# Kernel tuning notes

Hardware: AMD Instinct MI355X
Metric: run time of the kernel (lower is better)

## Reference

```python
import jax, jax.numpy as jnp
import numpy as np
from jax import lax
from jax.scipy.special import gammaln

B, T_FEATS, T_TEXT = 16, 2000, 400
ADIM, ODIM = 256, 512
BIG_NEG = -1e30
BLANK_LOGP = -1.0  # log(blank_prob) with blank_prob = e**-1


def _conv1d(x, w, b, pad):
    # x: (B, C_in, L), w: (C_out, C_in, K)
    y = lax.conv_general_dilated(x, w, (1,), [(pad, pad)],
                                 dimension_numbers=('NCH', 'OIH', 'NCH'))
    return y + b[None, :, None]


def _betabinom_prior(T, N):
    # ESPnet AlignmentModule beta-binomial attention prior (w=1):
    # alpha_t = t (1..T), beta_t = T - t + 1, k = 1..N, n = N
    t = jnp.arange(1, T + 1, dtype=jnp.float32)
    a = t[:, None]                                   # (T,1)
    bb = (T - t + 1.0)[:, None]                      # (T,1)
    k = jnp.arange(1, N + 1, dtype=jnp.float32)[None, :]  # (1,N)
    n = float(N)
    betaln = lambda x, y: gammaln(x) + gammaln(y) - gammaln(x + y)
    logC = gammaln(n + 1.0) - gammaln(k + 1.0) - gammaln(n - k + 1.0)
    return logC + betaln(k + a, n - k + bb) - betaln(a, bb)  # (T,N)


def _alignment_encoder(txt, speech, tw1, tb1, tw2, tb2, fw1, fb1, fw2, fb2, fw3, fb3):
    t = txt.transpose(0, 2, 1)                       # (B, adim, T_text)
    t = jax.nn.relu(_conv1d(t, tw1, tb1, 1))
    t = _conv1d(t, tw2, tb2, 0)
    t = t.transpose(0, 2, 1)                         # (B, T_text, adim)

    f = speech.transpose(0, 2, 1)                    # (B, odim, T_feats)
    f = jax.nn.relu(_conv1d(f, fw1, fb1, 1))
    f = jax.nn.relu(_conv1d(f, fw2, fb2, 1))
    f = _conv1d(f, fw3, fb3, 0)
    f = f.transpose(0, 2, 1)                         # (B, T_feats, adim)

    # score = -||f_t - t_s||_2 via expansion (avoids (B,T,S,D) intermediate)
    d2 = (jnp.sum(f * f, -1)[:, :, None] + jnp.sum(t * t, -1)[:, None, :]
          - 2.0 * jnp.einsum('btd,bsd->bts', f, t))
    score = -jnp.sqrt(jnp.maximum(d2, 1e-12))        # (B, T_feats, T_text)
    logp = jax.nn.log_softmax(score, axis=-1)
    return logp + _betabinom_prior(T_FEATS, T_TEXT)[None]


def _forwardsum_loss(log_p_attn):
    # CTC forward algorithm; targets are 1..N (all distinct) + interleaved blanks
    Bv, T, N = log_p_attn.shape
    lp = jnp.concatenate(
        [jnp.full((Bv, T, 1), BLANK_LOGP, log_p_attn.dtype), log_p_attn], axis=-1)
    lp = jax.nn.log_softmax(lp, axis=-1)             # (B, T, N+1)
    S = 2 * N + 1
    ext = np.zeros(S, np.int32); ext[1::2] = np.arange(1, N + 1)
    skip_ok = np.zeros(S, bool); skip_ok[3::2] = True  # non-blank, distinct labels
    ext = jnp.asarray(ext); skip_ok = jnp.asarray(skip_ok)

    emit = lp[:, :, ext]                             # (B, T, S)
    alpha = jnp.full((Bv, S), BIG_NEG)
    alpha = alpha.at[:, 0].set(emit[:, 0, 0]).at[:, 1].set(emit[:, 0, 1])

    def step(alpha, e):
        a1 = jnp.concatenate([jnp.full((Bv, 1), BIG_NEG), alpha[:, :-1]], axis=1)
        a2 = jnp.concatenate([jnp.full((Bv, 2), BIG_NEG), alpha[:, :-2]], axis=1)
        a2 = jnp.where(skip_ok[None, :], a2, BIG_NEG)
        alpha = jnp.logaddexp(jnp.logaddexp(alpha, a1), a2) + e
        return alpha, None

    alpha, _ = lax.scan(step, alpha, jnp.moveaxis(emit[:, 1:], 1, 0))
    nll = -jnp.logaddexp(alpha[:, -1], alpha[:, -2])  # (B,)
    # F.ctc_loss reduction='mean' divides each sample's nll by target length
    return jnp.mean(nll / N)


def _mas_single(lp):
    # lp: (T_feats, T_text) -> monotonic alignment (T_feats,) int32
    log_prob = lp.T                                  # (N, T)
    N, T = T_TEXT, T_FEATS
    q0 = jnp.where(jnp.arange(N) == 0, log_prob[0, 0], BIG_NEG)

    def fwd(q, col):
        q = jnp.maximum(q, jnp.concatenate([jnp.full((1,), BIG_NEG), q[:-1]])) + col
        return q, q

    _, qs = lax.scan(fwd, q0, log_prob[:, 1:].T)     # (T-1, N)
    Q = lax.stop_gradient(jnp.concatenate([q0[None], qs], axis=0))  # (T, N)

    def bwd(a_next, q_col):
        i_a = jnp.maximum(a_next - 1, 0)
        a = jnp.where(a_next == 0, 0,
                      jnp.where(q_col[i_a] >= q_col[a_next], i_a, a_next))
        a = a.astype(jnp.int32)
        return a, a

    _, A_rev = lax.scan(bwd, jnp.array(N - 1, jnp.int32), Q[:-1], reverse=True)
    return jnp.concatenate([A_rev, jnp.array([N - 1], jnp.int32)])  # (T,)


def _viterbi_decode(log_p_attn):
    A = jax.vmap(_mas_single)(log_p_attn)            # (B, T_feats) int32
    ds = jax.vmap(lambda a: jnp.bincount(a, length=T_TEXT))(A)
    ds = ds.astype(log_p_attn.dtype)                 # (B, T_text) durations
    gathered = jnp.take_along_axis(log_p_attn, A[:, :, None], axis=2)[..., 0]
    bin_loss = -jnp.mean(jnp.mean(gathered, axis=1))
    return ds, bin_loss


def setup_inputs() -> dict:
    key = jax.random.key(0)
    ks = jax.random.split(key, 12)
    s = 0.05
    inp = {
        'speech': jax.random.normal(ks[0], (B, T_FEATS, ODIM), jnp.float32),
        'txt': jax.random.normal(ks[1], (B, T_TEXT, ADIM), jnp.float32),
        'speech_len': jnp.full((B,), T_FEATS, jnp.int32),
        'txt_len': jnp.full((B,), T_TEXT, jnp.int32),
        'tw1': jax.random.normal(ks[2], (ADIM, ADIM, 3)) * s,
        'tb1': jnp.zeros((ADIM,)),
        'tw2': jax.random.normal(ks[3], (ADIM, ADIM, 1)) * s,
        'tb2': jnp.zeros((ADIM,)),
        'fw1': jax.random.normal(ks[4], (ADIM, ODIM, 3)) * s,
        'fb1': jnp.zeros((ADIM,)),
        'fw2': jax.random.normal(ks[5], (ADIM, ADIM, 3)) * s,
        'fb2': jnp.zeros((ADIM,)),
        'fw3': jax.random.normal(ks[6], (ADIM, ADIM, 1)) * s,
        'fb3': jnp.zeros((ADIM,)),
    }
    return inp


def reference(speech, txt, speech_len, txt_len,
              tw1, tb1, tw2, tb2, fw1, fb1, fw2, fb2, fw3, fb3):
    # lengths are full (no padding), so masks are no-ops
    log_p_attn = _alignment_encoder(txt, speech, tw1, tb1, tw2, tb2,
                                    fw1, fb1, fw2, fb2, fw3, fb3)
    forwardsum_loss = _forwardsum_loss(log_p_attn)
    ds, bin_loss = _viterbi_decode(log_p_attn)
    return ds, bin_loss, forwardsum_loss, log_p_attn
```

## Files before the change

### kernel.cpp

```cpp
#include <hip/hip_runtime.h>
#include <math.h>

typedef unsigned int u32;
typedef unsigned long long u64;
typedef unsigned short u16;
typedef __attribute__((ext_vector_type(8))) _Float16 f16x8;
typedef __attribute__((ext_vector_type(4))) float f32x4;

#define BIGN (-1e30f)

static constexpr int NB = 16;
static constexpr int TF = 2000;
static constexpr int TT = 400;

__device__ __forceinline__ float wsum(float v){
#pragma unroll
  for(int o=32;o;o>>=1) v += __shfl_xor(v,o,64);
  return v;
}
__device__ __forceinline__ float EXP2(float x){ return __builtin_amdgcn_exp2f(x); }
__device__ __forceinline__ float LOG2(float x){ return __builtin_amdgcn_logf(x); }
__device__ __forceinline__ float lse2b(float x, float y){
  float m = fmaxf(x,y);
  return m + LOG2(1.0f + EXP2(-fabsf(x-y)));
}
__device__ __forceinline__ float lse3b(float x, float y, float z){
  float mx = fmaxf(fmaxf(x,y),z);
  float md = __builtin_amdgcn_fmed3f(x,y,z);
  float mn = fminf(fminf(x,y),z);
  return mx + LOG2(1.0f + EXP2(md-mx) + EXP2(mn-mx));
}
__device__ __forceinline__ u16 f2h(float v){
  _Float16 h = (_Float16)v;
  return *(u16*)&h;
}
__device__ __forceinline__ float shup1(float v){
  int r = __builtin_amdgcn_update_dpp(__float_as_int(BIGN), __float_as_int(v),
                                      0x138, 0xf, 0xf, false);
  return __int_as_float(r);
}

__global__ void k_lgt(double* lgt){
  int m = blockIdx.x*blockDim.x + threadIdx.x;
  if(m < 2432) lgt[m] = (m>=1)? lgamma((double)m) : 0.0;
}
__global__ void k_terms(const double* __restrict__ lgt, double* rowA, double* colA, double* sA){
  int i = blockIdx.x*blockDim.x + threadIdx.x;
  if(i < TF)   rowA[i] = -lgt[2401] - lgt[i+1] - lgt[2000-i] + lgt[2001];
  if(i < TT)   colA[i] =  lgt[401]  - lgt[i+2] - lgt[400-i];
  if(i < 2399) sA[i]   =  lgt[i+2]  + lgt[2399-i];
}

__device__ __forceinline__ void packf(const float* __restrict__ w, u16* __restrict__ dst,
    int CIN, int KW, int i){
  int k = i % KW;
  int c = (i / KW) % CIN;
  int o = i / (KW*CIN);
  dst[((size_t)k*256 + o)*CIN + c] = f2h(w[i]);
}
__device__ __forceinline__ void cvtp(const float* __restrict__ src, u16* __restrict__ dst,
    int P, int C, int i){
  int c = i % C;
  int p = (i / C) % (P+2);
  int b = i / (C*(P+2));
  float v = 0.f;
  if(p>=1 && p<=P) v = src[((size_t)b*P + (p-1))*C + c];
  dst[i] = f2h(v);
}
__device__ __forceinline__ void zpr(u16* __restrict__ buf, int P, int j){
  int c = j % 256;
  int s = (j / 256) & 1;
  int b = j / 512;
  buf[((size_t)b*(P+2) + (s? P+1 : 0))*256 + c] = 0;
}
__global__ __launch_bounds__(256) void prep1_k(
    const float* __restrict__ fw1, const float* __restrict__ fw2, const float* __restrict__ fw3,
    const float* __restrict__ tw1, const float* __restrict__ tw2, const float* __restrict__ txt,
    u16* fw1p, u16* fw2p, u16* fw3p, u16* tw1p, u16* tw2p,
    u16* inbfT, u16* tout1, u16* out1){
  constexpr int N = 393216+196608+65536+196608+65536+1646592+8192+8192;
  for(int i = blockIdx.x*256 + threadIdx.x; i < N; i += gridDim.x*256){
    int j = i;
    if(j < 393216){ packf(fw1, fw1p, 512, 3, j); continue; } j -= 393216;
    if(j < 196608){ packf(fw2, fw2p, 256, 3, j); continue; } j -= 196608;
    if(j < 65536) { packf(fw3, fw3p, 256, 1, j); continue; } j -= 65536;
    if(j < 196608){ packf(tw1, tw1p, 256, 3, j); continue; } j -= 196608;
    if(j < 65536) { packf(tw2, tw2p, 256, 1, j); continue; } j -= 65536;
    if(j < 1646592){ cvtp(txt, inbfT, TT, 256, j); continue; } j -= 1646592;
    if(j < 8192) { zpr(tout1, TT, j); continue; } j -= 8192;
    zpr(out1, TF, j);
  }
}

__global__ __launch_bounds__(256) void cvt_pad_k(const float* __restrict__ src, u16* __restrict__ dst,
    int P, int C){
  int n = NB*(P+2)*C;
  for(int i = blockIdx.x*256 + threadIdx.x; i < n; i += gridDim.x*256) cvtp(src, dst, P, C, i);
}
__global__ __launch_bounds__(256) void zpad_k(u16* __restrict__ buf, int P){
  int n = NB*2*256;
  for(int i = blockIdx.x*256 + threadIdx.x; i < n; i += gridDim.x*256) zpr(buf, P, i);
}

template<int CIN, int KW, bool RELU, bool OBF>
__global__ __launch_bounds__(256) void mfconv_k(const u16* __restrict__ inb,
    const u16* __restrict__ wp, const float* __restrict__ bias, void* __restrict__ outp, int P){
  __shared__ __align__(16) u16 Al[4*66*8];
  __shared__ __align__(16) u16 Bl[KW*4*256*8];
  const int b = blockIdx.y;
  const int m0 = blockIdx.x * 64;
  const int tid = threadIdx.x;
  const int lane = tid & 63, wv = tid >> 6;
  const int lo16 = lane & 15, hi = lane >> 4;
  constexpr int K1 = (KW==1)? 1 : 0;
  const u16* inB = inb + (size_t)b*(P+2)*CIN;
  f32x4 acc[4][4];
#pragma unroll
  for(int i=0;i<4;i++)
#pragma unroll
    for(int j=0;j<4;j++) acc[i][j] = (f32x4){0.f,0.f,0.f,0.f};

  for(int c0=0; c0<CIN; c0+=32){
    __syncthreads();
    for(int idx = tid; idx < 264; idx += 256){
      int r = idx >> 2, q = idx & 3;
      int rowp = m0 + r;
      f16x8 v = (f16x8){0,0,0,0,0,0,0,0};
      if(rowp <= P+1) v = *(const f16x8*)&inB[(size_t)rowp*CIN + c0 + q*8];
      *(f16x8*)&Al[(q*66 + r)*8] = v;
    }
#pragma unroll
    for(int k=0;k<KW;k++){
      const u16* wr = &wp[((size_t)(k*256) + tid)*CIN + c0];
      f16x8 w0 = *(const f16x8*)&wr[0];
      f16x8 w1 = *(const f16x8*)&wr[8];
      f16x8 w2 = *(const f16x8*)&wr[16];
      f16x8 w3 = *(const f16x8*)&wr[24];
      *(f16x8*)&Bl[((k*4+0)*256 + tid)*8] = w0;
      *(f16x8*)&Bl[((k*4+1)*256 + tid)*8] = w1;
      *(f16x8*)&Bl[((k*4+2)*256 + tid)*8] = w2;
      *(f16x8*)&Bl[((k*4+3)*256 + tid)*8] = w3;
    }
    __syncthreads();
#pragma unroll
    for(int k=0;k<KW;k++){
      f16x8 af[4];
#pragma unroll
      for(int rf=0;rf<4;rf++)
        af[rf] = *(const f16x8*)&Al[(hi*66 + rf*16 + lo16 + k + K1)*8];
#pragma unroll
      for(int cf=0;cf<4;cf++){
        int o = wv*64 + cf*16 + lo16;
        f16x8 bf = *(const f16x8*)&Bl[((k*4+hi)*256 + o)*8];
#pragma unroll
        for(int rf=0;rf<4;rf++)
          acc[rf][cf] = __builtin_amdgcn_mfma_f32_16x16x32_f16(af[rf], bf, acc[rf][cf], 0, 0, 0);
      }
    }
  }
#pragma unroll
  for(int cf=0;cf<4;cf++){
    int o = wv*64 + cf*16 + lo16;
    float bs = bias[o];
#pragma unroll
    for(int rf=0;rf<4;rf++){
#pragma unroll
      for(int j=0;j<4;j++){
        int p = m0 + rf*16 + hi*4 + j;
        if(p < P){
          float v = acc[rf][cf][j] + bs;
          if(RELU) v = fmaxf(v, 0.f);
          if(OBF) ((u16*)outp)[((size_t)b*(P+2) + p + 1)*256 + o] = f2h(v);
          else    ((float*)outp)[((size_t)b*P + p)*256 + o] = v;
        }
      }
    }
  }
}

__global__ __launch_bounds__(256) void norm2b_k(const float* __restrict__ x1, const float* __restrict__ x2,
    float* __restrict__ o1, float* __restrict__ o2){
  int r = blockIdx.x*4 + (threadIdx.x>>6);
  int lane = threadIdx.x & 63;
  const float* src; float* dst; int rr;
  if(r < NB*TF){ src = x1; dst = o1; rr = r; }
  else { rr = r - NB*TF; if(rr >= NB*TT) return; src = x2; dst = o2; }
  float4 v = ((const float4*)(src + (size_t)rr*256))[lane];
  float s = v.x*v.x + v.y*v.y + v.z*v.z + v.w*v.w;
  s = wsum(s);
  if(lane==0) dst[rr] = s;
}

__global__ __launch_bounds__(256) void score_gemm(const float* __restrict__ F, const float* __restrict__ Tn,
    const float* __restrict__ fn2, const float* __restrict__ tn2, float* __restrict__ outp){
  constexpr int KC = 32;
  __shared__ __align__(16) float As[KC][68];
  __shared__ __align__(16) float Bs[KC][68];
  const int b = blockIdx.z;
  const int t0 = blockIdx.y*64, s0 = blockIdx.x*64;
  const int tid = threadIdx.x, tx = tid&15, ty = tid>>4;
  const float* Fb = F  + (size_t)b*TF*256;
  const float* Tb = Tn + (size_t)b*TT*256;
  float acc[4][4] = {};
  const int lk = tid & 31, lt0 = (tid>>5)*8;
  for(int k0=0;k0<256;k0+=KC){
    __syncthreads();
#pragma unroll
    for(int i=0;i<8;i++){
      int t = t0 + lt0 + i;
      As[lk][lt0+i] = (t<TF)? Fb[(size_t)t*256 + k0 + lk] : 0.f;
      int s = s0 + lt0 + i;
      Bs[lk][lt0+i] = (s<TT)? Tb[(size_t)s*256 + k0 + lk] : 0.f;
    }
    __syncthreads();
#pragma unroll
    for(int k=0;k<KC;k++){
      float a0[4], b0[4];
      *(float4*)a0 = *(const float4*)&As[k][ty*4];
      *(float4*)b0 = *(const float4*)&Bs[k][tx*4];
#pragma unroll
      for(int i=0;i<4;i++)
#pragma unroll
        for(int j=0;j<4;j++) acc[i][j] = fmaf(a0[i], b0[j], acc[i][j]);
    }
  }
#pragma unroll
  for(int i=0;i<4;i++){
    int t = t0 + ty*4 + i;
    if(t<TF){
      float fn = fn2[b*TF + t];
#pragma unroll
      for(int j=0;j<4;j++){
        int s = s0 + tx*4 + j;
        if(s<TT){
          float d2 = fn + tn2[b*TT + s] - 2.f*acc[i][j];
          outp[((size_t)b*TF + t)*TT + s] = -sqrtf(fmaxf(d2, 1e-12f));
        }
      }
    }
  }
}

__global__ __launch_bounds__(128) void softmax_prior_k(float* __restrict__ logp,
    const double* __restrict__ rowA, const double* __restrict__ colA, const double* __restrict__ sA,
    float* __restrict__ Z2){
  const int row = blockIdx.x;
  const int t0 = row % TF;
  float* rp = logp + (size_t)row*TT;
  const int tid = threadIdx.x;
  __shared__ float sh2[2];
  float v[4]; int ix[4];
#pragma unroll
  for(int i=0;i<4;i++){ ix[i] = tid + i*128; v[i] = (ix[i]<TT)? rp[ix[i]] : BIGN; }
  float m = fmaxf(fmaxf(v[0],v[1]),fmaxf(v[2],v[3]));
#pragma unroll
  for(int o=32;o;o>>=1) m = fmaxf(m, __shfl_xor(m,o,64));
  if((tid&63)==0) sh2[tid>>6] = m;
  __syncthreads();
  m = fmaxf(sh2[0], sh2[1]);
  float s = 0.f;
#pragma unroll
  for(int i=0;i<4;i++) if(ix[i]<TT) s += __expf(v[i]-m);
  s = wsum(s);
  __syncthreads();
  if((tid&63)==0) sh2[tid>>6] = s;
  __syncthreads();
  s = sh2[0] + sh2[1];
  const float lse = m + __logf(s);
  const double rA = rowA[t0];
  float f[4]; float m2 = BIGN;
#pragma unroll
  for(int i=0;i<4;i++){
    if(ix[i]<TT){
      float pr = (float)(colA[ix[i]] + sA[t0+ix[i]] + rA);
      f[i] = (v[i]-lse) + pr;
      rp[ix[i]] = f[i];
      m2 = fmaxf(m2, f[i]);
    } else f[i] = BIGN;
  }
#pragma unroll
  for(int o=32;o;o>>=1) m2 = fmaxf(m2, __shfl_xor(m2,o,64));
  __syncthreads();
  if((tid&63)==0) sh2[tid>>6] = m2;
  __syncthreads();
  m2 = fmaxf(fmaxf(sh2[0],sh2[1]), -1.0f);
  float s2 = (tid==0)? __expf(-1.0f - m2) : 0.f;
#pragma unroll
  for(int i=0;i<4;i++) if(ix[i]<TT) s2 += __expf(f[i]-m2);
  s2 = wsum(s2);
  __syncthreads();
  if((tid&63)==0) sh2[tid>>6] = s2;
  __syncthreads();
  if(tid==0) Z2[row] = m2 + __logf(sh2[0]+sh2[1]);
}

#define LCTC8(E) { \
  float n1 = shup1(a[7]); \
  float w0 = lse2b(a[0], n1); \
  float w1 = lse2b(a[2], a[1]); \
  float w2 = lse2b(a[4], a[3]); \
  float w3 = lse2b(a[6], a[5]); \
  a[7] = lse2b(a[7], w3) + (E)[3]; \
  a[5] = lse2b(a[5], w2) + (E)[2]; \
  a[3] = lse2b(a[3], w1) + (E)[1]; \
  a[1] = lse2b(a[1], w0) + (E)[0]; \
  a[6] = w3 + EBL; a[4] = w2 + EBL; a[2] = w1 + EBL; a[0] = w0 + EBL; }

#define CPREF4(E, K) { int kk=(K); if(kk>999) kk=999; int row = dir? (TF-1-kk) : kk; \
  const float* rpp = lp + (size_t)row*TT; \
  (E)[0]=rpp[jc[0]]*IL2; (E)[1]=rpp[jc[1]]*IL2; (E)[2]=rpp[jc[2]]*IL2; (E)[3]=rpp[jc[3]]*IL2; }

#define MAS_STEP(E, TIDX) { \
  float n1 = shup1(q[6]); \
  u32 byte = 0; \
  if(lane>0 && n1 >= q[0]) byte |= 1u; \
  if(q[0] >= q[1]) byte |= 2u; \
  if(q[1] >= q[2]) byte |= 4u; \
  if(q[2] >= q[3]) byte |= 8u; \
  if(q[3] >= q[4]) byte |= 16u; \
  if(q[4] >= q[5]) byte |= 32u; \
  if(q[5] >= q[6]) byte |= 64u; \
  cb[(size_t)((TIDX)-1)*64 + lane] = (unsigned char)byte; \
  q[6] = fmaxf(q[6], q[5]) + (E)[6]; \
  q[5] = fmaxf(q[5], q[4]) + (E)[5]; \
  q[4] = fmaxf(q[4], q[3]) + (E)[4]; \
  q[3] = fmaxf(q[3], q[2]) + (E)[3]; \
  q[2] = fmaxf(q[2], q[1]) + (E)[2]; \
  q[1] = fmaxf(q[1], q[0]) + (E)[1]; \
  q[0] = fmaxf(q[0], n1) + (E)[0]; }

#define MPREF(E, ROW) { int rr=(ROW); rr = (rr>TF-1)? (TF-1) : rr; const float* rpp = lp + (size_t)rr*TT; \
  (E)[0]=rpp[jc[0]]; (E)[1]=rpp[jc[1]]; (E)[2]=rpp[jc[2]]; (E)[3]=rpp[jc[3]]; \
  (E)[4]=rpp[jc[4]]; (E)[5]=rpp[jc[5]]; (E)[6]=rpp[jc[6]]; }

__global__ __launch_bounds__(256) __attribute__((amdgpu_waves_per_eu(1,1)))
void scan_k(const float* __restrict__ logp,
    const float* __restrict__ Z2, unsigned char* __restrict__ cmpb, float* __restrict__ nll){
  const int lane = threadIdx.x & 63;
  const int wave = threadIdx.x >> 6;
  constexpr float IL2 = 1.4426950408889634f;
  constexpr float L2  = 0.6931471805599453f;
  if(blockIdx.x < NB){
    const int b = blockIdx.x;
    const float* lp = logp + (size_t)b*TF*TT;
    __shared__ float af[801], ag[801];
    __shared__ float sb[2][2][16];
    const int dir  = wave >> 1;
    const int half = wave & 1;
    const int sbase = half ? 408 : 0;
    double zs = 0.0;
    if(wave==0){
      for(int t=lane; t<TF; t+=64) zs += (double)Z2[b*TF + t];
#pragma unroll
      for(int o=32;o;o>>=1) zs += __shfl_xor(zs, o, 64);
    }
    int jc[4];
#pragma unroll
    for(int i=0;i<4;i++){
      int j = sbase/2 + 4*lane + i;
      if(dir) j = TT-1-j;
      jc[i] = (j < 0)? 0 : ((j > TT-1)? TT-1 : j);
    }
    float a[8];
#pragma unroll
    for(int i=0;i<8;i++) a[i] = BIGN;
    if(half==0 && lane==0){
      a[0] = -1.0f*IL2;
      a[1] = (dir? lp[(size_t)(TF-1)*TT + (TT-1)] : lp[0]) * IL2;
    }
    const float EBL = -1.0f*IL2;
    if(half==0 && (lane==51 || lane==52)){
#pragma unroll
      for(int i=0;i<8;i++) sb[dir][0][(lane-51)*8+i] = a[i];
    }
    float e0[4],e1[4],e2[4],e3[4],e4[4],e5[4],e6[4],e7[4];
    CPREF4(e0,1); CPREF4(e1,2); CPREF4(e2,3); CPREF4(e3,4);
    CPREF4(e4,5); CPREF4(e5,6); CPREF4(e6,7); CPREF4(e7,8);
    __syncthreads();
    int k = 1, kb = 0;
    for(; k + 8 <= 1000; k += 8, kb++){
      if(half && lane < 2){
#pragma unroll
        for(int i=0;i<8;i++) a[i] = sb[dir][kb&1][lane*8+i];
      }
      LCTC8(e0); CPREF4(e0, k+8);
      LCTC8(e1); CPREF4(e1, k+9);
      LCTC8(e2); CPREF4(e2, k+10);
      LCTC8(e3); CPREF4(e3, k+11);
      LCTC8(e4); CPREF4(e4, k+12);
      LCTC8(e5); CPREF4(e5, k+13);
      LCTC8(e6); CPREF4(e6, k+14);
      LCTC8(e7); CPREF4(e7, k+15);
      if(half==0 && (lane==51 || lane==52)){
#pragma unroll
        for(int i=0;i<8;i++) sb[dir][(kb+1)&1][(lane-51)*8+i] = a[i];
      }
      __syncthreads();
    }
    if(half && lane < 2){
#pragma unroll
      for(int i=0;i<8;i++) a[i] = sb[dir][kb&1][lane*8+i];
    }
    for(; k<=999; k++){
      float P[4];
      CPREF4(P, k);
      LCTC8(P);
    }
    float* dst = dir? ag : af;
#pragma unroll
    for(int i=0;i<8;i++){
      int s = sbase + 8*lane + i;
      if(half){ if(s>=424 && s<=800) dst[s] = a[i]; }
      else    { if(s<=423) dst[s] = a[i]; }
    }
    __syncthreads();
    if(wave==0){
      float acc = BIGN;
      for(int s = lane; s <= 800; s += 64){
        float x0 = af[s];
        float x1 = (s>=1)? af[s-1] : BIGN;
        float x2 = ((s&1) && s>=3)? af[s-2] : BIGN;
        float A1 = lse3b(x0,x1,x2);
        acc = lse2b(acc, A1 + ag[800-s]);
      }
#pragma unroll
      for(int o=32;o;o>>=1) acc = lse2b(acc, __shfl_xor(acc,o,64));
      if(lane==0) nll[b] = -((acc*L2) - (float)zs);
    }
  } else {
    if(wave) return;
    const int b = blockIdx.x - NB;
    const float* lp = logp + (size_t)b*TF*TT;
    unsigned char* cb = cmpb + (size_t)b*TF*64;
    int jc[7];
#pragma unroll
    for(int i=0;i<7;i++){ int j = 7*lane + i; jc[i] = (j < TT)? j : (TT-1); }
    float q[7];
#pragma unroll
    for(int i=0;i<7;i++) q[i] = BIGN;
    if(lane==0) q[0] = lp[0];
    float e0[7],e1[7],e2[7],e3[7];
    MPREF(e0,1); MPREF(e1,2); MPREF(e2,3); MPREF(e3,4);
    int t0 = 1;
    for(; t0 + 4 <= TF; t0 += 4){
      MAS_STEP(e0, t0);   MPREF(e0, t0+4);
      MAS_STEP(e1, t0+1); MPREF(e1, t0+5);
      MAS_STEP(e2, t0+2); MPREF(e2, t0+6);
      MAS_STEP(e3, t0+3); MPREF(e3, t0+7);
    }
    for(; t0<TF; t0++){
      float P[7];
      MPREF(P, t0);
      MAS_STEP(P, t0);
    }
    {
      float n1 = shup1(q[6]);
      u32 byte = 0;
      if(lane>0 && n1 >= q[0]) byte |= 1u;
      if(q[0] >= q[1]) byte |= 2u;
      if(q[1] >= q[2]) byte |= 4u;
      if(q[2] >= q[3]) byte |= 8u;
      if(q[3] >= q[4]) byte |= 16u;
      if(q[4] >= q[5]) byte |= 32u;
      if(q[5] >= q[6]) byte |= 64u;
      cb[(size_t)(TF-1)*64 + lane] = (unsigned char)byte;
    }
  }
}

__global__ __launch_bounds__(256) void masback_k(const unsigned char* __restrict__ cmpb,
    const float* __restrict__ logp, float* __restrict__ ds, float* __restrict__ gsum){
  const int b = blockIdx.x;
  const unsigned char* cb = cmpb + (size_t)b*TF*64;
  __shared__ unsigned char bits[500*64];
  __shared__ short Ash[TF];
  __shared__ int cnt[TT];
  __shared__ float ps[4];
  int a = TT-1;
  for(int ch=3; ch>=0; ch--){
    const int tlo = ch*500;
    __syncthreads();
    for(int i=threadIdx.x;i<8000;i+=256) ((u32*)bits)[i] = ((const u32*)(cb + (size_t)tlo*64))[i];
    __syncthreads();
    if(threadIdx.x==0){
      int thi = tlo + 499;
      if(ch==3){ Ash[TF-1] = (short)(TT-1); thi = TF-2; }
      for(int t=thi;t>=tlo;t--){
        if(a > 0){
          unsigned char w = bits[(t-tlo)*64 + a/7];
          a -= (int)((w >> (a%7)) & 1u);
        }
        Ash[t] = (short)a;
      }
    }
  }
  __syncthreads();
  for(int i=threadIdx.x;i<TT;i+=256) cnt[i]=0;
  __syncthreads();
  float part = 0.f;
  const float* lp = logp + (size_t)b*TF*TT;
  for(int t=threadIdx.x;t<TF;t+=256){
    int at = Ash[t];
    atomicAdd(&cnt[at], 1);
    part += lp[(size_t)t*TT + at];
  }
  __syncthreads();
  for(int i=threadIdx.x;i<TT;i+=256) ds[(size_t)b*TT + i] = (float)cnt[i];
  part = wsum(part);
  if((threadIdx.x&63)==0) ps[threadIdx.x>>6] = part;
  __syncthreads();
  if(threadIdx.x==0) gsum[b] = ps[0]+ps[1]+ps[2]+ps[3];
}

__global__ void final_k(const float* __restrict__ nll, const float* __restrict__ gsum, float* __restrict__ out){
  if(threadIdx.x==0 && blockIdx.x==0){
    float fs=0.f, bs=0.f;
    for(int b=0;b<NB;b++){ fs += nll[b] / (float)TT; bs += gsum[b] / (float)TF; }
    out[6400] = -(bs / (float)NB);
    out[6401] = fs / (float)NB;
  }
}

extern "C" void kernel_launch(void* const* d_in, const int* in_sizes, int n_in,
                              void* d_out, int out_size, void* d_ws, size_t ws_size,
                              hipStream_t stream){
  const float* speech = (const float*)d_in[0];
  const float* txt    = (const float*)d_in[1];
  const float* tw1 = (const float*)d_in[4];
  const float* tb1 = (const float*)d_in[5];
  const float* tw2 = (const float*)d_in[6];
  const float* tb2 = (const float*)d_in[7];
  const float* fw1 = (const float*)d_in[8];
  const float* fb1 = (const float*)d_in[9];
  const float* fw2 = (const float*)d_in[10];
  const float* fb2 = (const float*)d_in[11];
  const float* fw3 = (const float*)d_in[12];
  const float* fb3 = (const float*)d_in[13];
  float* out  = (float*)d_out;
  float* ds   = out;
  float* logp = out + 6402;
  char* ws = (char*)d_ws;
  double* lgt  = (double*)(ws + 0);
  double* rowA = (double*)(ws + 20480);
  double* colA = (double*)(ws + 36864);
  double* sA   = (double*)(ws + 40960);
  float*  nll  = (float*)(ws + 61440);
  float*  gsum = (float*)(ws + 61696);
  float*  Z2   = (float*)(ws + 65536);
  float*  fn2  = (float*)(ws + 196608);
  float*  tn2  = (float*)(ws + 327680);
  unsigned char* cmpb = (unsigned char*)(ws + 360448);
  float*  tenc = (float*)(ws + 2408448);
  float*  f1   = (float*)(ws + 8962048);
  if(ws_size < 41730048) return;

  char* lr = (char*)(((uintptr_t)logp + 255) & ~(uintptr_t)255);
  u16* inbfT = (u16*)lr;
  u16* tout1 = (u16*)(lr + 4000000);
  u16* inbfA = (u16*)lr;
  u16* out2  = (u16*)lr;
  u16* wbase = (u16*)(lr + 32900000);
  u16* fw1p = wbase;
  u16* fw2p = wbase + 393216;
  u16* fw3p = wbase + 589824;
  u16* tw1p = wbase + 655360;
  u16* tw2p = wbase + 851968;
  u16* out1  = (u16*)(lr + 34750000);

  k_lgt  <<<10,256,0,stream>>>(lgt);
  k_terms<<<10,256,0,stream>>>(lgt,rowA,colA,sA);

  prep1_k<<<2048,256,0,stream>>>(fw1,fw2,fw3,tw1,tw2, txt,
                                 fw1p,fw2p,fw3p,tw1p,tw2p, inbfT, tout1, out1);

  mfconv_k<256,3,true ,true ><<<dim3(7,NB),256,0,stream>>>(inbfT, tw1p, tb1, tout1, TT);
  mfconv_k<256,1,false,false><<<dim3(7,NB),256,0,stream>>>(tout1, tw2p, tb2, tenc, TT);

  cvt_pad_k<<<4096,256,0,stream>>>(speech, inbfA, TF, 512);
  mfconv_k<512,3,true ,true ><<<dim3(32,NB),256,0,stream>>>(inbfA, fw1p, fb1, out1, TF);
  zpad_k<<<32,256,0,stream>>>(out2, TF);
  mfconv_k<256,3,true ,true ><<<dim3(32,NB),256,0,stream>>>(out1, fw2p, fb2, out2, TF);
  mfconv_k<256,1,false,false><<<dim3(32,NB),256,0,stream>>>(out2, fw3p, fb3, f1, TF);

  norm2b_k<<<(NB*TF+NB*TT)/4,256,0,stream>>>(f1, tenc, fn2, tn2);

  score_gemm<<<dim3(7,32,NB),256,0,stream>>>(f1, tenc, fn2, tn2, logp);
  softmax_prior_k<<<NB*TF,128,0,stream>>>(logp, rowA, colA, sA, Z2);

  scan_k<<<2*NB,256,0,stream>>>(logp, Z2, cmpb, nll);
  masback_k<<<NB,256,0,stream>>>(cmpb, logp, ds, gsum);
  final_k<<<1,64,0,stream>>>(nll, gsum, out);
}
```

Before: 819.2 us.

## Interleave two batches per wave in scan kernel to hide serial latency

Each scan block now runs two independent batch recurrences interleaved in the same waves: 8 blocks each carry two CTC forward-backward problems and 8 blocks each carry two Viterbi/MAS chains. The grid drops from 32 to 16 blocks. The aim is to give each wave two independent dependency chains so shuffle, exp/log and load latencies of one can overlap with the other in this latency-bound serial scan. The cost is more register pressure and more instructions per step per wave, so if the scan is throughput-bound the kernel could slow down.

```diff
diff --git a/kernel.cpp b/kernel.cpp
--- a/kernel.cpp
+++ b/kernel.cpp
@@ -294,42 +294,43 @@
   if(tid==0) Z2[row] = m2 + __logf(sh2[0]+sh2[1]);
 }
 
-#define LCTC8(E) { \
-  float n1 = shup1(a[7]); \
-  float w0 = lse2b(a[0], n1); \
-  float w1 = lse2b(a[2], a[1]); \
-  float w2 = lse2b(a[4], a[3]); \
-  float w3 = lse2b(a[6], a[5]); \
-  a[7] = lse2b(a[7], w3) + (E)[3]; \
-  a[5] = lse2b(a[5], w2) + (E)[2]; \
-  a[3] = lse2b(a[3], w1) + (E)[1]; \
-  a[1] = lse2b(a[1], w0) + (E)[0]; \
-  a[6] = w3 + EBL; a[4] = w2 + EBL; a[2] = w1 + EBL; a[0] = w0 + EBL; }
-
-#define CPREF4(E, K) { int kk=(K); if(kk>999) kk=999; int row = dir? (TF-1-kk) : kk; \
-  const float* rpp = lp + (size_t)row*TT; \
+#define LCTC8(A, E) { \
+  float n1 = shup1(A[7]); \
+  float w0 = lse2b(A[0], n1); \
+  float w1 = lse2b(A[2], A[1]); \
+  float w2 = lse2b(A[4], A[3]); \
+  float w3 = lse2b(A[6], A[5]); \
+  A[7] = lse2b(A[7], w3) + (E)[3]; \
+  A[5] = lse2b(A[5], w2) + (E)[2]; \
+  A[3] = lse2b(A[3], w1) + (E)[1]; \
+  A[1] = lse2b(A[1], w0) + (E)[0]; \
+  A[6] = w3 + EBL; A[4] = w2 + EBL; A[2] = w1 + EBL; A[0] = w0 + EBL; }
+
+#define CPREF4(E, LP, K) { int kk=(K); if(kk>999) kk=999; int row = dir? (TF-1-kk) : kk; \
+  const float* rpp = (LP) + (size_t)row*TT; \
   (E)[0]=rpp[jc[0]]*IL2; (E)[1]=rpp[jc[1]]*IL2; (E)[2]=rpp[jc[2]]*IL2; (E)[3]=rpp[jc[3]]*IL2; }
 
-#define MAS_STEP(E, TIDX) { \
-  float n1 = shup1(q[6]); \
+#define MAS_STEP(Q, E, CB, TIDX) { \
+  float n1 = shup1(Q[6]); \
   u32 byte = 0; \
-  if(lane>0 && n1 >= q[0]) byte |= 1u; \
-  if(q[0] >= q[1]) byte |= 2u; \
-  if(q[1] >= q[2]) byte |= 4u; \
-  if(q[2] >= q[3]) byte |= 8u; \
-  if(q[3] >= q[4]) byte |= 16u; \
-  if(q[4] >= q[5]) byte |= 32u; \
-  if(q[5] >= q[6]) byte |= 64u; \
-  cb[(size_t)((TIDX)-1)*64 + lane] = (unsigned char)byte; \
-  q[6] = fmaxf(q[6], q[5]) + (E)[6]; \
-  q[5] = fmaxf(q[5], q[4]) + (E)[5]; \
-  q[4] = fmaxf(q[4], q[3]) + (E)[4]; \
-  q[3] = fmaxf(q[3], q[2]) + (E)[3]; \
-  q[2] = fmaxf(q[2], q[1]) + (E)[2]; \
-  q[1] = fmaxf(q[1], q[0]) + (E)[1]; \
-  q[0] = fmaxf(q[0], n1) + (E)[0]; }
-
-#define MPREF(E, ROW) { int rr=(ROW); rr = (rr>TF-1)? (TF-1) : rr; const float* rpp = lp + (size_t)rr*TT; \
+  if(lane>0 && n1 >= Q[0]) byte |= 1u; \
+  if(Q[0] >= Q[1]) byte |= 2u; \
+  if(Q[1] >= Q[2]) byte |= 4u; \
+  if(Q[2] >= Q[3]) byte |= 8u; \
+  if(Q[3] >= Q[4]) byte |= 16u; \
+  if(Q[4] >= Q[5]) byte |= 32u; \
+  if(Q[5] >= Q[6]) byte |= 64u; \
+  (CB)[(size_t)((TIDX)-1)*64 + lane] = (unsigned char)byte; \
+  Q[6] = fmaxf(Q[6], Q[5]) + (E)[6]; \
+  Q[5] = fmaxf(Q[5], Q[4]) + (E)[5]; \
+  Q[4] = fmaxf(Q[4], Q[3]) + (E)[4]; \
+  Q[3] = fmaxf(Q[3], Q[2]) + (E)[3]; \
+  Q[2] = fmaxf(Q[2], Q[1]) + (E)[2]; \
+  Q[1] = fmaxf(Q[1], Q[0]) + (E)[1]; \
+  Q[0] = fmaxf(Q[0], n1) + (E)[0]; }
+
+#define MPREF(E, LP, ROW) { int rr=(ROW); rr = (rr>TF-1)? (TF-1) : rr; \
+  const float* rpp = (LP) + (size_t)rr*TT; \
   (E)[0]=rpp[jc[0]]; (E)[1]=rpp[jc[1]]; (E)[2]=rpp[jc[2]]; (E)[3]=rpp[jc[3]]; \
   (E)[4]=rpp[jc[4]]; (E)[5]=rpp[jc[5]]; (E)[6]=rpp[jc[6]]; }
 
@@ -340,19 +341,20 @@
   const int wave = threadIdx.x >> 6;
   constexpr float IL2 = 1.4426950408889634f;
   constexpr float L2  = 0.6931471805599453f;
-  if(blockIdx.x < NB){
-    const int b = blockIdx.x;
-    const float* lp = logp + (size_t)b*TF*TT;
-    __shared__ float af[801], ag[801];
-    __shared__ float sb[2][2][16];
+  if(blockIdx.x < 8){
+    const int bA = blockIdx.x, bB = blockIdx.x + 8;
+    const float* lpA = logp + (size_t)bA*TF*TT;
+    const float* lpB = logp + (size_t)bB*TF*TT;
+    __shared__ float af[2][801], ag[2][801];
+    __shared__ float sb[2][2][2][16];
     const int dir  = wave >> 1;
     const int half = wave & 1;
     const int sbase = half ? 408 : 0;
-    double zs = 0.0;
+    double zsA = 0.0, zsB = 0.0;
     if(wave==0){
-      for(int t=lane; t<TF; t+=64) zs += (double)Z2[b*TF + t];
-#pragma unroll
-      for(int o=32;o;o>>=1) zs += __shfl_xor(zs, o, 64);
+      for(int t=lane; t<TF; t+=64){ zsA += (double)Z2[bA*TF + t]; zsB += (double)Z2[bB*TF + t]; }
+#pragma unroll
+      for(int o=32;o;o>>=1){ zsA += __shfl_xor(zsA, o, 64); zsB += __shfl_xor(zsB, o, 64); }
     }
     int jc[4];
 #pragma unroll
@@ -361,109 +363,148 @@
       if(dir) j = TT-1-j;
       jc[i] = (j < 0)? 0 : ((j > TT-1)? TT-1 : j);
     }
-    float a[8];
-#pragma unroll
-    for(int i=0;i<8;i++) a[i] = BIGN;
+    float aA[8], aB[8];
+#pragma unroll
+    for(int i=0;i<8;i++){ aA[i] = BIGN; aB[i] = BIGN; }
     if(half==0 && lane==0){
-      a[0] = -1.0f*IL2;
-      a[1] = (dir? lp[(size_t)(TF-1)*TT + (TT-1)] : lp[0]) * IL2;
+      aA[0] = -1.0f*IL2;
+      aA[1] = (dir? lpA[(size_t)(TF-1)*TT + (TT-1)] : lpA[0]) * IL2;
+      aB[0] = -1.0f*IL2;
+      aB[1] = (dir? lpB[(size_t)(TF-1)*TT + (TT-1)] : lpB[0]) * IL2;
     }
     const float EBL = -1.0f*IL2;
     if(half==0 && (lane==51 || lane==52)){
 #pragma unroll
-      for(int i=0;i<8;i++) sb[dir][0][(lane-51)*8+i] = a[i];
-    }
-    float e0[4],e1[4],e2[4],e3[4],e4[4],e5[4],e6[4],e7[4];
-    CPREF4(e0,1); CPREF4(e1,2); CPREF4(e2,3); CPREF4(e3,4);
-    CPREF4(e4,5); CPREF4(e5,6); CPREF4(e6,7); CPREF4(e7,8);
+      for(int i=0;i<8;i++){
+        sb[0][dir][0][(lane-51)*8+i] = aA[i];
+        sb[1][dir][0][(lane-51)*8+i] = aB[i];
+      }
+    }
+    float eA0[4],eA1[4],eA2[4],eA3[4],eA4[4],eA5[4],eA6[4],eA7[4];
+    float eB0[4],eB1[4],eB2[4],eB3[4],eB4[4],eB5[4],eB6[4],eB7[4];
+    CPREF4(eA0,lpA,1); CPREF4(eA1,lpA,2); CPREF4(eA2,lpA,3); CPREF4(eA3,lpA,4);
+    CPREF4(eA4,lpA,5); CPREF4(eA5,lpA,6); CPREF4(eA6,lpA,7); CPREF4(eA7,lpA,8);
+    CPREF4(eB0,lpB,1); CPREF4(eB1,lpB,2); CPREF4(eB2,lpB,3); CPREF4(eB3,lpB,4);
+    CPREF4(eB4,lpB,5); CPREF4(eB5,lpB,6); CPREF4(eB6,lpB,7); CPREF4(eB7,lpB,8);
     __syncthreads();
     int k = 1, kb = 0;
     for(; k + 8 <= 1000; k += 8, kb++){
       if(half && lane < 2){
 #pragma unroll
-        for(int i=0;i<8;i++) a[i] = sb[dir][kb&1][lane*8+i];
-      }
-      LCTC8(e0); CPREF4(e0, k+8);
-      LCTC8(e1); CPREF4(e1, k+9);
-      LCTC8(e2); CPREF4(e2, k+10);
-      LCTC8(e3); CPREF4(e3, k+11);
-      LCTC8(e4); CPREF4(e4, k+12);
-      LCTC8(e5); CPREF4(e5, k+13);
-      LCTC8(e6); CPREF4(e6, k+14);
-      LCTC8(e7); CPREF4(e7, k+15);
+        for(int i=0;i<8;i++){
+          aA[i] = sb[0][dir][kb&1][lane*8+i];
+          aB[i] = sb[1][dir][kb&1][lane*8+i];
+        }
+      }
+      LCTC8(aA,eA0); LCTC8(aB,eB0); CPREF4(eA0,lpA,k+8);  CPREF4(eB0,lpB,k+8);
+      LCTC8(aA,eA1); LCTC8(aB,eB1); CPREF4(eA1,lpA,k+9);  CPREF4(eB1,lpB,k+9);
+      LCTC8(aA,eA2); LCTC8(aB,eB2); CPREF4(eA2,lpA,k+10); CPREF4(eB2,lpB,k+10);
+      LCTC8(aA,eA3); LCTC8(aB,eB3); CPREF4(eA3,lpA,k+11); CPREF4(eB3,lpB,k+11);
+      LCTC8(aA,eA4); LCTC8(aB,eB4); CPREF4(eA4,lpA,k+12); CPREF4(eB4,lpB,k+12);
+      LCTC8(aA,eA5); LCTC8(aB,eB5); CPREF4(eA5,lpA,k+13); CPREF4(eB5,lpB,k+13);
+      LCTC8(aA,eA6); LCTC8(aB,eB6); CPREF4(eA6,lpA,k+14); CPREF4(eB6,lpB,k+14);
+      LCTC8(aA,eA7); LCTC8(aB,eB7); CPREF4(eA7,lpA,k+15); CPREF4(eB7,lpB,k+15);
       if(half==0 && (lane==51 || lane==52)){
 #pragma unroll
-        for(int i=0;i<8;i++) sb[dir][(kb+1)&1][(lane-51)*8+i] = a[i];
+        for(int i=0;i<8;i++){
+          sb[0][dir][(kb+1)&1][(lane-51)*8+i] = aA[i];
+          sb[1][dir][(kb+1)&1][(lane-51)*8+i] = aB[i];
+        }
       }
       __syncthreads();
     }
     if(half && lane < 2){
 #pragma unroll
-      for(int i=0;i<8;i++) a[i] = sb[dir][kb&1][lane*8+i];
+      for(int i=0;i<8;i++){
+        aA[i] = sb[0][dir][kb&1][lane*8+i];
+        aB[i] = sb[1][dir][kb&1][lane*8+i];
+      }
     }
     for(; k<=999; k++){
-      float P[4];
-      CPREF4(P, k);
-      LCTC8(P);
-    }
-    float* dst = dir? ag : af;
+      float PA[4], PB[4];
+      CPREF4(PA,lpA,k); CPREF4(PB,lpB,k);
+      LCTC8(aA,PA); LCTC8(aB,PB);
+    }
+    float* dstA = dir? ag[0] : af[0];
+    float* dstB = dir? ag[1] : af[1];
 #pragma unroll
     for(int i=0;i<8;i++){
       int s = sbase + 8*lane + i;
-      if(half){ if(s>=424 && s<=800) dst[s] = a[i]; }
-      else    { if(s<=423) dst[s] = a[i]; }
+      bool ok = half ? (s>=424 && s<=800) : (s<=423);
+      if(ok){ dstA[s] = aA[i]; dstB[s] = aB[i]; }
     }
     __syncthreads();
     if(wave==0){
-      float acc = BIGN;
+      float accA = BIGN, accB = BIGN;
       for(int s = lane; s <= 800; s += 64){
-        float x0 = af[s];
-        float x1 = (s>=1)? af[s-1] : BIGN;
-        float x2 = ((s&1) && s>=3)? af[s-2] : BIGN;
-        float A1 = lse3b(x0,x1,x2);
-        acc = lse2b(acc, A1 + ag[800-s]);
-      }
-#pragma unroll
-      for(int o=32;o;o>>=1) acc = lse2b(acc, __shfl_xor(acc,o,64));
-      if(lane==0) nll[b] = -((acc*L2) - (float)zs);
+        float x1A = (s>=1)? af[0][s-1] : BIGN;
+        float x2A = ((s&1) && s>=3)? af[0][s-2] : BIGN;
+        accA = lse2b(accA, lse3b(af[0][s],x1A,x2A) + ag[0][800-s]);
+        float x1B = (s>=1)? af[1][s-1] : BIGN;
+        float x2B = ((s&1) && s>=3)? af[1][s-2] : BIGN;
+        accB = lse2b(accB, lse3b(af[1][s],x1B,x2B) + ag[1][800-s]);
+      }
+#pragma unroll
+      for(int o=32;o;o>>=1){
+        accA = lse2b(accA, __shfl_xor(accA,o,64));
+        accB = lse2b(accB, __shfl_xor(accB,o,64));
+      }
+      if(lane==0){
+        nll[bA] = -((accA*L2) - (float)zsA);
+        nll[bB] = -((accB*L2) - (float)zsB);
+      }
     }
   } else {
     if(wave) return;
-    const int b = blockIdx.x - NB;
-    const float* lp = logp + (size_t)b*TF*TT;
-    unsigned char* cb = cmpb + (size_t)b*TF*64;
+    const int bA = blockIdx.x - 8, bB = blockIdx.x;
+    const float* lpA = logp + (size_t)bA*TF*TT;
+    const float* lpB = logp + (size_t)bB*TF*TT;
+    unsigned char* cbA = cmpb + (size_t)bA*TF*64;
+    unsigned char* cbB = cmpb + (size_t)bB*TF*64;
     int jc[7];
 #pragma unroll
     for(int i=0;i<7;i++){ int j = 7*lane + i; jc[i] = (j < TT)? j : (TT-1); }
-    float q[7];
-#pragma unroll
-    for(int i=0;i<7;i++) q[i] = BIGN;
-    if(lane==0) q[0] = lp[0];
-    float e0[7],e1[7],e2[7],e3[7];
-    MPREF(e0,1); MPREF(e1,2); MPREF(e2,3); MPREF(e3,4);
+    float qA[7], qB[7];
+#pragma unroll
+    for(int i=0;i<7;i++){ qA[i] = BIGN; qB[i] = BIGN; }
+    if(lane==0){ qA[0] = lpA[0]; qB[0] = lpB[0]; }
+    float eA0[7],eA1[7],eA2[7],eA3[7];
+    float eB0[7],eB1[7],eB2[7],eB3[7];
+    MPREF(eA0,lpA,1); MPREF(eA1,lpA,2); MPREF(eA2,lpA,3); MPREF(eA3,lpA,4);
+    MPREF(eB0,lpB,1); MPREF(eB1,lpB,2); MPREF(eB2,lpB,3); MPREF(eB3,lpB,4);
     int t0 = 1;
     for(; t0 + 4 <= TF; t0 += 4){
-      MAS_STEP(e0, t0);   MPREF(e0, t0+4);
-      MAS_STEP(e1, t0+1); MPREF(e1, t0+5);
-      MAS_STEP(e2, t0+2); MPREF(e2, t0+6);
-      MAS_STEP(e3, t0+3); MPREF(e3, t0+7);
+      MAS_STEP(qA,eA0,cbA,t0);   MAS_STEP(qB,eB0,cbB,t0);   MPREF(eA0,lpA,t0+4); MPREF(eB0,lpB,t0+4);
+      MAS_STEP(qA,eA1,cbA,t0+1); MAS_STEP(qB,eB1,cbB,t0+1); MPREF(eA1,lpA,t0+5); MPREF(eB1,lpB,t0+5);
+      MAS_STEP(qA,eA2,cbA,t0+2); MAS_STEP(qB,eB2,cbB,t0+2); MPREF(eA2,lpA,t0+6); MPREF(eB2,lpB,t0+6);
+      MAS_STEP(qA,eA3,cbA,t0+3); MAS_STEP(qB,eB3,cbB,t0+3); MPREF(eA3,lpA,t0+7); MPREF(eB3,lpB,t0+7);
     }
     for(; t0<TF; t0++){
-      float P[7];
-      MPREF(P, t0);
-      MAS_STEP(P, t0);
+      float PA[7], PB[7];
+      MPREF(PA,lpA,t0); MPREF(PB,lpB,t0);
+      MAS_STEP(qA,PA,cbA,t0); MAS_STEP(qB,PB,cbB,t0);
     }
     {
-      float n1 = shup1(q[6]);
-      u32 byte = 0;
-      if(lane>0 && n1 >= q[0]) byte |= 1u;
-      if(q[0] >= q[1]) byte |= 2u;
-      if(q[1] >= q[2]) byte |= 4u;
-      if(q[2] >= q[3]) byte |= 8u;
-      if(q[3] >= q[4]) byte |= 16u;
-      if(q[4] >= q[5]) byte |= 32u;
-      if(q[5] >= q[6]) byte |= 64u;
-      cb[(size_t)(TF-1)*64 + lane] = (unsigned char)byte;
+      float n1A = shup1(qA[6]);
+      u32 byteA = 0;
+      if(lane>0 && n1A >= qA[0]) byteA |= 1u;
+      if(qA[0] >= qA[1]) byteA |= 2u;
+      if(qA[1] >= qA[2]) byteA |= 4u;
+      if(qA[2] >= qA[3]) byteA |= 8u;
+      if(qA[3] >= qA[4]) byteA |= 16u;
+      if(qA[4] >= qA[5]) byteA |= 32u;
+      if(qA[5] >= qA[6]) byteA |= 64u;
+      cbA[(size_t)(TF-1)*64 + lane] = (unsigned char)byteA;
+      float n1B = shup1(qB[6]);
+      u32 byteB = 0;
+      if(lane>0 && n1B >= qB[0]) byteB |= 1u;
+      if(qB[0] >= qB[1]) byteB |= 2u;
+      if(qB[1] >= qB[2]) byteB |= 4u;
+      if(qB[2] >= qB[3]) byteB |= 8u;
+      if(qB[3] >= qB[4]) byteB |= 16u;
+      if(qB[4] >= qB[5]) byteB |= 32u;
+      if(qB[5] >= qB[6]) byteB |= 64u;
+      cbB[(size_t)(TF-1)*64 + lane] = (unsigned char)byteB;
     }
   }
 }
@@ -587,7 +628,7 @@
   score_gemm<<<dim3(7,32,NB),256,0,stream>>>(f1, tenc, fn2, tn2, logp);
   softmax_prior_k<<<NB*TF,128,0,stream>>>(logp, rowA, colA, sA, Z2);
 
-  scan_k<<<2*NB,256,0,stream>>>(logp, Z2, cmpb, nll);
+  scan_k<<<16,256,0,stream>>>(logp, Z2, cmpb, nll);
   masback_k<<<NB,256,0,stream>>>(cmpb, logp, ds, gsum);
   final_k<<<1,64,0,stream>>>(nll, gsum, out);
 }
```

Result: slower. 1.080 ms (+31.9%).
